# Optimization experiments

Measured on AMD Instinct MI355X. Metric: run time of the kernel, lower is better.

Reference implementation:

```python
import jax, jax.numpy as jnp
import numpy as np

B, L, E = 512, 50, 512
VOCAB = 32000
EPS = 1e-5


def setup_inputs() -> dict:
    key = jax.random.key(0)
    ks = jax.random.split(key, 16)
    inp = {
        'src_tokens': jax.random.randint(ks[0], (B, L), 0, VOCAB, dtype=jnp.int32),
        'trg_tokens': jax.random.randint(ks[1], (B, L), 0, VOCAB, dtype=jnp.int32),
        'pad_idx': 1,
        'emb_src': jax.random.normal(ks[2], (VOCAB, E), jnp.float32) * 0.02,
        'emb_trg': jax.random.normal(ks[3], (VOCAB, E), jnp.float32) * 0.02,
        'W1': jax.random.normal(ks[4], (20, E), jnp.float32) / np.sqrt(E),  # Conv1d(1,20,k=E) kernel squeezed
        'b1': jax.random.normal(ks[5], (20,), jnp.float32) * 0.01,
        'g1': jnp.ones((20,), jnp.float32),
        'beta1': jnp.zeros((20,), jnp.float32),
        'W2': jax.random.normal(ks[6], (40, 20, 3, 3), jnp.float32) / np.sqrt(20 * 9),
        'b2': jax.random.normal(ks[7], (40,), jnp.float32) * 0.01,
        'g2': jnp.ones((40,), jnp.float32),
        'beta2': jnp.zeros((40,), jnp.float32),
        'Wfc1': jax.random.normal(ks[8], (20, 40 * 11 * 11), jnp.float32) / np.sqrt(40 * 11 * 11),
        'bfc1': jnp.zeros((20,), jnp.float32),
        'Wfc2': jax.random.normal(ks[9], (1, 20), jnp.float32) / np.sqrt(20),
        'bfc2': jnp.zeros((1,), jnp.float32),
    }
    return inp


def _maxpool2(x):  # [B,C,H,W] -> 2x2/2 valid max pool
    return jax.lax.reduce_window(x, -jnp.inf, jax.lax.max, (1, 1, 2, 2), (1, 1, 2, 2), 'VALID')


def reference(src_tokens, trg_tokens, pad_idx, emb_src, emb_trg, W1, b1, g1, beta1,
              W2, b2, g2, beta2, Wfc1, bfc1, Wfc2, bfc2):
    src_e = emb_src[src_tokens]  # [B,L,E]
    trg_e = emb_trg[trg_tokens]  # [B,L,E]

    def conv1_bn_relu(x):
        # per-sample Conv1d(1,20,k=E): collapses E -> scalar per position/channel
        f = jnp.einsum('ble,ce->blc', x, W1) + b1  # [B,L,20]
        # per-sample BatchNorm1d in training mode: stats over the L positions of each sample
        mu = jnp.mean(f, axis=1, keepdims=True)
        var = jnp.var(f, axis=1, keepdims=True)  # biased, as torch uses for normalization
        f = (f - mu) * jax.lax.rsqrt(var + EPS) * g1 + beta1
        return jax.nn.relu(f)

    s = conv1_bn_relu(src_e)  # [B,L,20]
    t = conv1_bn_relu(trg_e)  # [B,L,20]

    # broadcast outer-sum: out[b,i,j,c] = s[b,j,c] + t[b,i,c]
    out = s[:, None, :, :] + t[:, :, None, :]          # [B,L,L,20]
    out = jnp.transpose(out, (0, 3, 1, 2))             # [B,20,L,L]
    out = _maxpool2(out)                                # [B,20,25,25]

    out = jax.lax.conv_general_dilated(out, W2, (1, 1), 'VALID') + b2[None, :, None, None]  # [B,40,23,23]
    # BatchNorm2d training mode: stats over (batch, H, W)
    mu = jnp.mean(out, axis=(0, 2, 3), keepdims=True)
    var = jnp.var(out, axis=(0, 2, 3), keepdims=True)
    out = (out - mu) * jax.lax.rsqrt(var + EPS) * g2[None, :, None, None] + beta2[None, :, None, None]
    out = jax.nn.relu(out)
    out = _maxpool2(out)                                # [B,40,11,11]

    out = out.reshape(out.shape[0], -1)                 # [B,4840]
    out = out @ Wfc1.T + bfc1
    out = out @ Wfc2.T + bfc2
    return jax.nn.sigmoid(out)                          # [B,1]
```

## Files before the change

### kernel.cpp

```cpp
#include <hip/hip_runtime.h>
#include <hip/hip_bf16.h>

#define EPS 1e-5f

__device__ __forceinline__ float bf2f(unsigned short u) {
  union { unsigned int i; float f; } x; x.i = ((unsigned int)u) << 16; return x.f;
}
__device__ __forceinline__ float loadp(const void* p, int i, bool f32) {
  return f32 ? ((const float*)p)[i] : bf2f(((const unsigned short*)p)[i]);
}
__device__ __forceinline__ bool detect_f32(const void* g1) {
  return ((const unsigned int*)g1)[0] == 0x3F800000u;
}

__global__ __launch_bounds__(256) void k0_prep(
    const void* __restrict__ W1, const void* __restrict__ W2,
    const void* __restrict__ Wfc1,
    const void* __restrict__ g1, const void* __restrict__ beta1,
    const void* __restrict__ g2, const void* __restrict__ beta2,
    const void* __restrict__ bfc1, const void* __restrict__ Wfc2,
    const void* __restrict__ bfc2,
    float* __restrict__ W1T, float* __restrict__ WT, float* __restrict__ WS,
    float* __restrict__ Wfc1T, float* __restrict__ prm)
{
  const bool f32 = detect_f32(g1);
  int g = blockIdx.x * 256 + threadIdx.x;
  const int NT = 64 * 256;
  for (int i = g; i < 512 * 20; i += NT) {
    int e = i / 20, c = i - e * 20;
    W1T[i] = loadp(W1, c * 512 + e, f32);
  }
  for (int i = g; i < 40 * 3 * 20; i += NT) {
    int o = i / 60, r = i - o * 60;
    int k = r / 20, c = r - k * 20;
    float st = 0.f, ss = 0.f;
    for (int q = 0; q < 3; ++q) {
      st += loadp(W2, ((o * 20 + c) * 3 + k) * 3 + q, f32);
      ss += loadp(W2, ((o * 20 + c) * 3 + q) * 3 + k, f32);
    }
    WT[(o * 3 + k) * 20 + c] = st;
    WS[(o * 3 + k) * 20 + c] = ss;
  }
  for (int i = g; i < 4840 * 20; i += NT) {
    int kk = i / 4840, idx = i - kk * 4840;
    Wfc1T[idx * 20 + kk] = loadp(Wfc1, i, f32);
  }
  if (g < 20)        prm[g] = loadp(g1,    g,       f32);
  else if (g < 40)   prm[g] = loadp(beta1, g - 20,  f32);
  else if (g < 80)   prm[g] = loadp(g2,    g - 40,  f32);
  else if (g < 120)  prm[g] = loadp(beta2, g - 80,  f32);
  else if (g < 140)  prm[g] = loadp(bfc1,  g - 120, f32);
  else if (g < 160)  prm[g] = loadp(Wfc2,  g - 140, f32);
  else if (g == 160) prm[g] = loadp(bfc2,  0,       f32);
}

__global__ __launch_bounds__(512) void k12_fused(
    const int* __restrict__ src_tok, const int* __restrict__ trg_tok,
    const void* __restrict__ emb_src, const void* __restrict__ emb_trg,
    const void* __restrict__ g1flag,
    const float* __restrict__ W1T,
    const float* __restrict__ WT, const float* __restrict__ WS,
    const float* __restrict__ prm,
    float* __restrict__ C1, float* __restrict__ R, float* __restrict__ S2)
{
  __shared__ float part[8 * 64 * 21];
  __shared__ float fl[1000];
  __shared__ float wl[2400];
  __shared__ float pmax[500];
  __shared__ float convl[40 * 24];
  __shared__ float sc[20], sh[20];
  const bool f32 = detect_f32(g1flag);
  int bb = blockIdx.x;
  int side = bb >> 9, b = bb & 511;
  int t = threadIdx.x;
  int lane = t & 63;
  int ch = __builtin_amdgcn_readfirstlane(t >> 6);

  float acc[20];
#pragma unroll
  for (int c = 0; c < 20; ++c) acc[c] = 0.f;
  if (lane < 50) {
    int tok = side ? trg_tok[b * 50 + lane] : src_tok[b * 50 + lane];
    const void* emb = side ? emb_trg : emb_src;
    if (f32) {
      const float4* rowp = (const float4*)((const float*)emb + (size_t)tok * 512 + ch * 64);
      for (int half = 0; half < 2; ++half) {
        float4 u[8];
#pragma unroll
        for (int q = 0; q < 8; ++q) u[q] = rowp[half * 8 + q];
#pragma unroll
        for (int q = 0; q < 8; ++q) {
          float v[4] = { u[q].x, u[q].y, u[q].z, u[q].w };
          const float* w = W1T + (ch * 64 + half * 32 + q * 4) * 20;
#pragma unroll
          for (int j = 0; j < 4; ++j)
#pragma unroll
            for (int c = 0; c < 20; ++c) acc[c] = fmaf(v[j], w[j * 20 + c], acc[c]);
        }
      }
    } else {
      const uint4* rowp = (const uint4*)((const unsigned short*)emb + (size_t)tok * 512 + ch * 64);
      uint4 u[8];
#pragma unroll
      for (int q = 0; q < 8; ++q) u[q] = rowp[q];
#pragma unroll
      for (int q = 0; q < 8; ++q) {
        const unsigned int* qu = (const unsigned int*)&u[q];
        float v[8];
#pragma unroll
        for (int j = 0; j < 4; ++j) {
          union { unsigned int i; float f; } lo, hi;
          lo.i = qu[j] << 16; hi.i = qu[j] & 0xffff0000u;
          v[2 * j] = lo.f; v[2 * j + 1] = hi.f;
        }
        const float* w = W1T + (ch * 64 + q * 8) * 20;
#pragma unroll
        for (int j = 0; j < 8; ++j)
#pragma unroll
          for (int c = 0; c < 20; ++c) acc[c] = fmaf(v[j], w[j * 20 + c], acc[c]);
      }
    }
    float* pp = &part[(ch * 64 + lane) * 21];
#pragma unroll
    for (int c = 0; c < 20; ++c) pp[c] = acc[c];
  }
  {
    const float* wsrc = side ? WT : WS;
    for (int i = t; i < 2400; i += 512) wl[i] = wsrc[i];
  }
  __syncthreads();
  for (int i = t; i < 1000; i += 512) {
    int l = i / 20, c = i - l * 20;
    float s = 0.f;
#pragma unroll
    for (int c2 = 0; c2 < 8; ++c2) s += part[(c2 * 64 + l) * 21 + c];
    fl[i] = s;
  }
  __syncthreads();
  if (t < 20) {
    float s = 0.f, s2 = 0.f;
#pragma unroll
    for (int l = 0; l < 50; ++l) { float v = fl[l * 20 + t]; s += v; s2 += v * v; }
    float mu = s * (1.0f / 50.0f);
    float var = s2 * (1.0f / 50.0f) - mu * mu;
    float k = prm[t] * rsqrtf(var + EPS);
    sc[t] = k; sh[t] = prm[20 + t] - k * mu;
  }
  __syncthreads();
  for (int i = t; i < 500; i += 512) {
    int p = i / 20, c = i - p * 20;
    float k = sc[c], s0 = sh[c];
    float v0 = fmaxf(k * fl[(2 * p) * 20 + c] + s0, 0.f);
    float v1 = fmaxf(k * fl[(2 * p + 1) * 20 + c] + s0, 0.f);
    pmax[i] = fmaxf(v0, v1);
  }
  __syncthreads();
  for (int i = t; i < 920; i += 512) {
    int o = i / 23, y = i - o * 23;
    float a = 0.f;
#pragma unroll
    for (int ky = 0; ky < 3; ++ky) {
      const float* wr = &wl[(o * 3 + ky) * 20];
      const float* pr = &pmax[(y + ky) * 20];
#pragma unroll
      for (int c = 0; c < 20; ++c) a = fmaf(wr[c], pr[c], a);
    }
    C1[((size_t)o * 1024 + bb) * 23 + y] = a;
    convl[o * 24 + y] = a;
  }
  __syncthreads();
  if (t < 40) {
    float s = 0.f, s2 = 0.f;
#pragma unroll
    for (int y = 0; y < 23; ++y) { float v = convl[t * 24 + y]; s += v; s2 += v * v; }
    R[t * 1024 + bb] = s;
    S2[t * 1024 + bb] = s2;
  }
}

__global__ __launch_bounds__(256) void k3_bn2(
    const float* __restrict__ R, const float* __restrict__ S2,
    const float* __restrict__ prm,
    float* __restrict__ bn2)
{
  int o = blockIdx.x, t = threadIdx.x;
  float s1a = 0, s2a = 0, s1b = 0, s2b = 0, sab = 0;
  for (int b = t; b < 512; b += 256) {
    float ra = R[o * 1024 + 512 + b], rb = R[o * 1024 + b];
    s1a += ra; s1b += rb; sab += ra * rb;
    s2a += S2[o * 1024 + 512 + b];
    s2b += S2[o * 1024 + b];
  }
  __shared__ float Rd[5][256];
  Rd[0][t] = s1a; Rd[1][t] = s2a; Rd[2][t] = s1b; Rd[3][t] = s2b; Rd[4][t] = sab;
  __syncthreads();
  for (int s = 128; s > 0; s >>= 1) {
    if (t < s) {
#pragma unroll
      for (int q = 0; q < 5; ++q) Rd[q][t] += Rd[q][t + s];
    }
    __syncthreads();
  }
  if (t == 0) {
    const float invN = 1.0f / (512.0f * 23.0f);
    float muA = Rd[0][0] * invN, muB = Rd[2][0] * invN;
    float ea2 = Rd[1][0] * invN - muA * muA;
    float eb2 = Rd[3][0] * invN - muB * muB;
    float cross = 2.0f * (Rd[4][0] * (1.0f / (529.0f * 512.0f)) - muA * muB);
    float var = ea2 + eb2 + cross;
    float k = prm[40 + o] * rsqrtf(var + EPS);
    bn2[o] = k;
    bn2[40 + o] = prm[80 + o] - k * (muA + muB);
  }
}

__global__ __launch_bounds__(256) void k4_fc(
    const float* __restrict__ C1,
    const float* __restrict__ bn2,
    const float* __restrict__ Wfc1T,
    const float* __restrict__ prm,
    const void* __restrict__ g1flag,
    void* __restrict__ outv)
{
  const bool f32 = detect_f32(g1flag);
  int b = blockIdx.x, t = threadIdx.x;
  __shared__ float mA[440], mB[440];
  __shared__ float k2s[40], c2s[40];
  __shared__ float red[20][256];
  __shared__ float o1[20];
  if (t < 40) k2s[t] = bn2[t];
  else if (t < 80) c2s[t - 40] = bn2[t];
  __syncthreads();
  for (int i = t; i < 440; i += 256) {
    int o = i / 11, y = i - o * 11;
    const float* pa = C1 + ((size_t)o * 1024 + 512 + b) * 23;
    const float* pb = C1 + ((size_t)o * 1024 + b) * 23;
    float a0 = pa[2 * y], a1 = pa[2 * y + 1];
    float b0 = pb[2 * y], b1 = pb[2 * y + 1];
    if (k2s[o] >= 0.f) { mA[i] = fmaxf(a0, a1); mB[i] = fmaxf(b0, b1); }
    else               { mA[i] = fminf(a0, a1); mB[i] = fminf(b0, b1); }
  }
  __syncthreads();
  float acc[20];
#pragma unroll
  for (int c = 0; c < 20; ++c) acc[c] = 0.f;
  for (int idx = t; idx < 4840; idx += 256) {
    int o = idx / 121, r = idx - o * 121;
    int y = r / 11, x = r - y * 11;
    float p = fmaxf(k2s[o] * (mA[o * 11 + y] + mB[o * 11 + x]) + c2s[o], 0.f);
    const float* w = Wfc1T + idx * 20;
#pragma unroll
    for (int c = 0; c < 20; ++c) acc[c] = fmaf(p, w[c], acc[c]);
  }
#pragma unroll
  for (int c = 0; c < 20; ++c) red[c][t] = acc[c];
  __syncthreads();
  for (int s = 128; s > 0; s >>= 1) {
    if (t < s) {
#pragma unroll
      for (int c = 0; c < 20; ++c) red[c][t] += red[c][t + s];
    }
    __syncthreads();
  }
  if (t < 20) o1[t] = red[t][0] + prm[120 + t];
  __syncthreads();
  if (t == 0) {
    float z = prm[160];
#pragma unroll
    for (int c = 0; c < 20; ++c) z = fmaf(prm[140 + c], o1[c], z);
    float sg = 1.0f / (1.0f + expf(-z));
    if (f32) ((float*)outv)[b] = sg;
    else     ((__hip_bfloat16*)outv)[b] = __float2bfloat16(sg);
  }
}

extern "C" void kernel_launch(void* const* d_in, const int* in_sizes, int n_in,
                              void* d_out, int out_size, void* d_ws, size_t ws_size,
                              hipStream_t stream) {
  const int* src_tok = (const int*)d_in[0];
  const int* trg_tok = (const int*)d_in[1];
  const void* emb_src = d_in[3];
  const void* emb_trg = d_in[4];
  const void* W1    = d_in[5];
  const void* g1    = d_in[7];
  const void* beta1 = d_in[8];
  const void* W2    = d_in[9];
  const void* g2    = d_in[11];
  const void* beta2 = d_in[12];
  const void* Wfc1  = d_in[13];
  const void* bfc1  = d_in[14];
  const void* Wfc2  = d_in[15];
  const void* bfc2  = d_in[16];

  char* ws = (char*)d_ws;
  float* W1T   = (float*)(ws + 0);
  float* WT    = (float*)(ws + 40960);
  float* WS    = (float*)(ws + 50560);
  float* Wfc1T = (float*)(ws + 60160);
  float* prm   = (float*)(ws + 447360);
  float* bn2   = (float*)(ws + 448384);
  float* R     = (float*)(ws + 448896);
  float* S2    = (float*)(ws + 612736);
  float* C1    = (float*)(ws + 776576);

  k0_prep<<<64, 256, 0, stream>>>(W1, W2, Wfc1, g1, beta1, g2, beta2, bfc1, Wfc2,
                                  bfc2, W1T, WT, WS, Wfc1T, prm);
  k12_fused<<<1024, 512, 0, stream>>>(src_tok, trg_tok, emb_src, emb_trg, g1,
                                      W1T, WT, WS, prm, C1, R, S2);
  k3_bn2<<<40, 256, 0, stream>>>(R, S2, prm, bn2);
  k4_fc<<<512, 256, 0, stream>>>(C1, bn2, Wfc1T, prm, g1, d_out);
}
```

Measured before the change: 202.8 us.

## Use bf16 MFMA for embedding-conv projection and halve block size

Adds a bf16 path that computes the embedding-by-W1 projection with 32x32x16 MFMA instructions, using a pre-packed W1 fragment buffer built in the prep kernel. The block shrinks from 512 to 256 threads. The f32 path is restructured so each of 4 waves handles 128 embedding elements, with a two-stage shared-memory reduction. The MFMA path targets the scalar FMA cost of the bf16 case. The f32 path trades parallelism per block for lower reduction and sync overhead.

```diff
diff --git a/kernel.cpp b/kernel.cpp
--- a/kernel.cpp
+++ b/kernel.cpp
@@ -2,6 +2,9 @@
 #include <hip/hip_bf16.h>
 
 #define EPS 1e-5f
+
+typedef __attribute__((ext_vector_type(8)))  short bf16x8;
+typedef __attribute__((ext_vector_type(16))) float f32x16;
 
 __device__ __forceinline__ float bf2f(unsigned short u) {
   union { unsigned int i; float f; } x; x.i = ((unsigned int)u) << 16; return x.f;
@@ -21,7 +24,8 @@
     const void* __restrict__ bfc1, const void* __restrict__ Wfc2,
     const void* __restrict__ bfc2,
     float* __restrict__ W1T, float* __restrict__ WT, float* __restrict__ WS,
-    float* __restrict__ Wfc1T, float* __restrict__ prm)
+    float* __restrict__ Wfc1T, float* __restrict__ prm,
+    unsigned short* __restrict__ Bp)
 {
   const bool f32 = detect_f32(g1);
   int g = blockIdx.x * 256 + threadIdx.x;
@@ -30,6 +34,16 @@
     int e = i / 20, c = i - e * 20;
     W1T[i] = loadp(W1, c * 512 + e, f32);
   }
+  const unsigned short* W1u = (const unsigned short*)W1;
+  for (int i = g; i < 2048; i += NT) {
+    int s = i >> 6, lane = i & 63;
+    int n = lane & 31, hk = lane >> 5;
+#pragma unroll
+    for (int j = 0; j < 8; ++j) {
+      int e = s * 16 + hk * 8 + j;
+      Bp[i * 8 + j] = (n < 20) ? W1u[n * 512 + e] : (unsigned short)0;
+    }
+  }
   for (int i = g; i < 40 * 3 * 20; i += NT) {
     int o = i / 60, r = i - o * 60;
     int k = r / 20, c = r - k * 20;
@@ -54,16 +68,17 @@
   else if (g == 160) prm[g] = loadp(bfc2,  0,       f32);
 }
 
-__global__ __launch_bounds__(512) void k12_fused(
+__global__ __launch_bounds__(256) void k12_fused(
     const int* __restrict__ src_tok, const int* __restrict__ trg_tok,
     const void* __restrict__ emb_src, const void* __restrict__ emb_trg,
     const void* __restrict__ g1flag,
     const float* __restrict__ W1T,
+    const unsigned short* __restrict__ Bp,
     const float* __restrict__ WT, const float* __restrict__ WS,
     const float* __restrict__ prm,
     float* __restrict__ C1, float* __restrict__ R, float* __restrict__ S2)
 {
-  __shared__ float part[8 * 64 * 21];
+  __shared__ float part[4 * 64 * 17];
   __shared__ float fl[1000];
   __shared__ float wl[2400];
   __shared__ float pmax[500];
@@ -74,69 +89,101 @@
   int side = bb >> 9, b = bb & 511;
   int t = threadIdx.x;
   int lane = t & 63;
-  int ch = __builtin_amdgcn_readfirstlane(t >> 6);
-
-  float acc[20];
-#pragma unroll
-  for (int c = 0; c < 20; ++c) acc[c] = 0.f;
-  if (lane < 50) {
-    int tok = side ? trg_tok[b * 50 + lane] : src_tok[b * 50 + lane];
-    const void* emb = side ? emb_trg : emb_src;
-    if (f32) {
-      const float4* rowp = (const float4*)((const float*)emb + (size_t)tok * 512 + ch * 64);
-      for (int half = 0; half < 2; ++half) {
+  int wave = __builtin_amdgcn_readfirstlane(t >> 6);
+
+  {
+    const float* wsrc = side ? WT : WS;
+    for (int i = t; i < 2400; i += 256) wl[i] = wsrc[i];
+  }
+
+  if (!f32) {
+    int tile = wave >> 1, kh = wave & 1;
+    int m = lane & 31, half = lane >> 5;
+    int grow = tile * 32 + m;
+    int lrow = grow < 50 ? grow : 49;
+    int tok = side ? trg_tok[b * 50 + lrow] : src_tok[b * 50 + lrow];
+    const unsigned short* arow =
+        (const unsigned short*)(side ? emb_trg : emb_src) + (size_t)tok * 512 + half * 8;
+    const unsigned short* bbase = Bp + ((size_t)(kh * 16) * 64 + lane) * 8;
+    f32x16 acc;
+#pragma unroll
+    for (int r = 0; r < 16; ++r) acc[r] = 0.f;
+    int s0 = kh * 16;
+#pragma unroll
+    for (int batch = 0; batch < 4; ++batch) {
+      uint4 ua[4], ub[4];
+#pragma unroll
+      for (int r = 0; r < 4; ++r) {
+        int s = s0 + batch * 4 + r;
+        ua[r] = *(const uint4*)(arow + s * 16);
+        ub[r] = *(const uint4*)(bbase + (batch * 4 + r) * 512);
+      }
+#pragma unroll
+      for (int r = 0; r < 4; ++r) {
+        union { uint4 u; bf16x8 h; } a, bfr;
+        a.u = ua[r]; bfr.u = ub[r];
+        acc = __builtin_amdgcn_mfma_f32_32x32x16_bf16(a.h, bfr.h, acc, 0, 0, 0);
+      }
+    }
+    float* pp = &part[wave * 1088 + lane * 17];
+#pragma unroll
+    for (int r = 0; r < 16; ++r) pp[r] = acc[r];
+    __syncthreads();
+    if (t < 128) {
+      int tl = t >> 6, ln = t & 63;
+      int c = ln & 31;
+#pragma unroll
+      for (int reg = 0; reg < 16; ++reg) {
+        float v = part[(tl * 2) * 1088 + ln * 17 + reg] +
+                  part[(tl * 2 + 1) * 1088 + ln * 17 + reg];
+        int row = (reg & 3) + 8 * (reg >> 2) + 4 * (ln >> 5);
+        int gr = tl * 32 + row;
+        if (c < 20 && gr < 50) fl[gr * 20 + c] = v;
+      }
+    }
+    __syncthreads();
+  } else {
+    float acc[20];
+#pragma unroll
+    for (int c = 0; c < 20; ++c) acc[c] = 0.f;
+    if (lane < 50) {
+      int tok = side ? trg_tok[b * 50 + lane] : src_tok[b * 50 + lane];
+      const float4* rowp = (const float4*)((const float*)(side ? emb_trg : emb_src) +
+                                           (size_t)tok * 512 + wave * 128);
+      for (int q8 = 0; q8 < 4; ++q8) {
         float4 u[8];
 #pragma unroll
-        for (int q = 0; q < 8; ++q) u[q] = rowp[half * 8 + q];
+        for (int q = 0; q < 8; ++q) u[q] = rowp[q8 * 8 + q];
 #pragma unroll
         for (int q = 0; q < 8; ++q) {
           float v[4] = { u[q].x, u[q].y, u[q].z, u[q].w };
-          const float* w = W1T + (ch * 64 + half * 32 + q * 4) * 20;
+          const float* w = W1T + (wave * 128 + q8 * 32 + q * 4) * 20;
 #pragma unroll
           for (int j = 0; j < 4; ++j)
 #pragma unroll
             for (int c = 0; c < 20; ++c) acc[c] = fmaf(v[j], w[j * 20 + c], acc[c]);
         }
       }
-    } else {
-      const uint4* rowp = (const uint4*)((const unsigned short*)emb + (size_t)tok * 512 + ch * 64);
-      uint4 u[8];
-#pragma unroll
-      for (int q = 0; q < 8; ++q) u[q] = rowp[q];
-#pragma unroll
-      for (int q = 0; q < 8; ++q) {
-        const unsigned int* qu = (const unsigned int*)&u[q];
-        float v[8];
-#pragma unroll
-        for (int j = 0; j < 4; ++j) {
-          union { unsigned int i; float f; } lo, hi;
-          lo.i = qu[j] << 16; hi.i = qu[j] & 0xffff0000u;
-          v[2 * j] = lo.f; v[2 * j + 1] = hi.f;
-        }
-        const float* w = W1T + (ch * 64 + q * 8) * 20;
-#pragma unroll
-        for (int j = 0; j < 8; ++j)
-#pragma unroll
-          for (int c = 0; c < 20; ++c) acc[c] = fmaf(v[j], w[j * 20 + c], acc[c]);
-      }
-    }
-    float* pp = &part[(ch * 64 + lane) * 21];
-#pragma unroll
-    for (int c = 0; c < 20; ++c) pp[c] = acc[c];
-  }
-  {
-    const float* wsrc = side ? WT : WS;
-    for (int i = t; i < 2400; i += 512) wl[i] = wsrc[i];
-  }
-  __syncthreads();
-  for (int i = t; i < 1000; i += 512) {
-    int l = i / 20, c = i - l * 20;
-    float s = 0.f;
-#pragma unroll
-    for (int c2 = 0; c2 < 8; ++c2) s += part[(c2 * 64 + l) * 21 + c];
-    fl[i] = s;
-  }
-  __syncthreads();
+    }
+    if (wave < 2 && lane < 50) {
+      float* pp = &part[(wave * 64 + lane) * 21];
+#pragma unroll
+      for (int c = 0; c < 20; ++c) pp[c] = acc[c];
+    }
+    __syncthreads();
+    if (wave >= 2 && lane < 50) {
+      float* pp = &part[((wave - 2) * 64 + lane) * 21];
+#pragma unroll
+      for (int c = 0; c < 20; ++c) pp[c] += acc[c];
+    }
+    __syncthreads();
+    for (int i = t; i < 1000; i += 256) {
+      int l = i / 20, c = i - l * 20;
+      fl[i] = part[(l) * 21 + c] + part[(64 + l) * 21 + c];
+    }
+    __syncthreads();
+  }
+
   if (t < 20) {
     float s = 0.f, s2 = 0.f;
 #pragma unroll
@@ -147,15 +194,15 @@
     sc[t] = k; sh[t] = prm[20 + t] - k * mu;
   }
   __syncthreads();
-  for (int i = t; i < 500; i += 512) {
+  for (int i = t; i < 500; i += 256) {
     int p = i / 20, c = i - p * 20;
-    float k = sc[c], s0 = sh[c];
-    float v0 = fmaxf(k * fl[(2 * p) * 20 + c] + s0, 0.f);
-    float v1 = fmaxf(k * fl[(2 * p + 1) * 20 + c] + s0, 0.f);
+    float k = sc[c], s0v = sh[c];
+    float v0 = fmaxf(k * fl[(2 * p) * 20 + c] + s0v, 0.f);
+    float v1 = fmaxf(k * fl[(2 * p + 1) * 20 + c] + s0v, 0.f);
     pmax[i] = fmaxf(v0, v1);
   }
   __syncthreads();
-  for (int i = t; i < 920; i += 512) {
+  for (int i = t; i < 920; i += 256) {
     int o = i / 23, y = i - o * 23;
     float a = 0.f;
 #pragma unroll
@@ -293,20 +340,21 @@
   const void* bfc2  = d_in[16];
 
   char* ws = (char*)d_ws;
-  float* W1T   = (float*)(ws + 0);
-  float* WT    = (float*)(ws + 40960);
-  float* WS    = (float*)(ws + 50560);
-  float* Wfc1T = (float*)(ws + 60160);
-  float* prm   = (float*)(ws + 447360);
-  float* bn2   = (float*)(ws + 448384);
-  float* R     = (float*)(ws + 448896);
-  float* S2    = (float*)(ws + 612736);
-  float* C1    = (float*)(ws + 776576);
+  float* W1T          = (float*)(ws + 0);
+  float* WT           = (float*)(ws + 40960);
+  float* WS           = (float*)(ws + 50560);
+  float* Wfc1T        = (float*)(ws + 60160);
+  float* prm          = (float*)(ws + 447360);
+  float* bn2          = (float*)(ws + 448384);
+  float* R            = (float*)(ws + 448896);
+  float* S2           = (float*)(ws + 612736);
+  unsigned short* Bp  = (unsigned short*)(ws + 776576);
+  float* C1           = (float*)(ws + 809344);
 
   k0_prep<<<64, 256, 0, stream>>>(W1, W2, Wfc1, g1, beta1, g2, beta2, bfc1, Wfc2,
-                                  bfc2, W1T, WT, WS, Wfc1T, prm);
-  k12_fused<<<1024, 512, 0, stream>>>(src_tok, trg_tok, emb_src, emb_trg, g1,
-                                      W1T, WT, WS, prm, C1, R, S2);
+                                  bfc2, W1T, WT, WS, Wfc1T, prm, Bp);
+  k12_fused<<<1024, 256, 0, stream>>>(src_tok, trg_tok, emb_src, emb_trg, g1,
+                                      W1T, Bp, WT, WS, prm, C1, R, S2);
   k3_bn2<<<40, 256, 0, stream>>>(R, S2, prm, bn2);
   k4_fc<<<512, 256, 0, stream>>>(C1, bn2, Wfc1T, prm, g1, d_out);
 }
```

Result: slower. 215.8 us (+6.4%).

## Precompute conv1 projection for whole vocabulary, then gather per token

Applied to the files above, without the earlier changes.

Splits the fused kernel in two. The first projects every row of both embedding tables through W1 into a compact bf16 table with 24-element rows. The second gathers those 20-value rows per token instead of gathering full 512-wide embedding rows and reducing them per sample. This trades random full-row gathers and partially idle lanes for a fully streaming pass over both tables. That pass touches more rows in total (the full vocabulary rather than only the tokens used) and rounds the projected features to bf16, which adds precision loss.

```diff
diff --git a/kernel.cpp b/kernel.cpp
--- a/kernel.cpp
+++ b/kernel.cpp
@@ -54,87 +54,113 @@
   else if (g == 160) prm[g] = loadp(bfc2,  0,       f32);
 }
 
-__global__ __launch_bounds__(512) void k12_fused(
-    const int* __restrict__ src_tok, const int* __restrict__ trg_tok,
+__global__ __launch_bounds__(256) void k1_vocab(
     const void* __restrict__ emb_src, const void* __restrict__ emb_trg,
     const void* __restrict__ g1flag,
     const float* __restrict__ W1T,
+    unsigned short* __restrict__ F)
+{
+  __shared__ float part[128 * 21];
+  const bool f32 = detect_f32(g1flag);
+  int t = threadIdx.x;
+  int slot = t & 127;
+  int kh = __builtin_amdgcn_readfirstlane(t >> 7);
+  int grow = blockIdx.x * 128 + slot;
+  int table = grow >= 32000;
+  int v = grow - table * 32000;
+  const void* emb = table ? emb_trg : emb_src;
+  float acc[20];
+#pragma unroll
+  for (int c = 0; c < 20; ++c) acc[c] = 0.f;
+  if (!f32) {
+    const uint4* rowp = (const uint4*)((const unsigned short*)emb + (size_t)v * 512 + kh * 256);
+    for (int outer = 0; outer < 4; ++outer) {
+      uint4 u[8];
+#pragma unroll
+      for (int q = 0; q < 8; ++q) u[q] = rowp[outer * 8 + q];
+#pragma unroll
+      for (int q = 0; q < 8; ++q) {
+        const unsigned int* qu = (const unsigned int*)&u[q];
+        float vv[8];
+#pragma unroll
+        for (int j = 0; j < 4; ++j) {
+          union { unsigned int i; float f; } lo, hi;
+          lo.i = qu[j] << 16; hi.i = qu[j] & 0xffff0000u;
+          vv[2 * j] = lo.f; vv[2 * j + 1] = hi.f;
+        }
+        const float* w = W1T + (kh * 256 + outer * 64 + q * 8) * 20;
+#pragma unroll
+        for (int j = 0; j < 8; ++j)
+#pragma unroll
+          for (int c = 0; c < 20; ++c) acc[c] = fmaf(vv[j], w[j * 20 + c], acc[c]);
+      }
+    }
+  } else {
+    const float4* rowp = (const float4*)((const float*)emb + (size_t)v * 512 + kh * 256);
+    for (int outer = 0; outer < 8; ++outer) {
+      float4 u[8];
+#pragma unroll
+      for (int q = 0; q < 8; ++q) u[q] = rowp[outer * 8 + q];
+#pragma unroll
+      for (int q = 0; q < 8; ++q) {
+        float vv[4] = { u[q].x, u[q].y, u[q].z, u[q].w };
+        const float* w = W1T + (kh * 256 + outer * 32 + q * 4) * 20;
+#pragma unroll
+        for (int j = 0; j < 4; ++j)
+#pragma unroll
+          for (int c = 0; c < 20; ++c) acc[c] = fmaf(vv[j], w[j * 20 + c], acc[c]);
+      }
+    }
+  }
+  if (kh == 0) {
+    float* pp = &part[slot * 21];
+#pragma unroll
+    for (int c = 0; c < 20; ++c) pp[c] = acc[c];
+  }
+  __syncthreads();
+  if (kh == 1) {
+    float* pp = &part[slot * 21];
+#pragma unroll
+    for (int c = 0; c < 20; ++c) pp[c] += acc[c];
+  }
+  __syncthreads();
+  for (int i = t; i < 2560; i += 256) {
+    int row = i / 20, c = i - row * 20;
+    float val = part[row * 21 + c];
+    F[(size_t)(blockIdx.x * 128 + row) * 24 + c] =
+        (unsigned short)(__bfloat16_as_ushort(__float2bfloat16(val)));
+  }
+}
+
+__global__ __launch_bounds__(256) void k2_sample(
+    const int* __restrict__ src_tok, const int* __restrict__ trg_tok,
+    const unsigned short* __restrict__ F,
     const float* __restrict__ WT, const float* __restrict__ WS,
     const float* __restrict__ prm,
     float* __restrict__ C1, float* __restrict__ R, float* __restrict__ S2)
 {
-  __shared__ float part[8 * 64 * 21];
   __shared__ float fl[1000];
   __shared__ float wl[2400];
   __shared__ float pmax[500];
   __shared__ float convl[40 * 24];
   __shared__ float sc[20], sh[20];
-  const bool f32 = detect_f32(g1flag);
+  __shared__ int tokl[50];
   int bb = blockIdx.x;
   int side = bb >> 9, b = bb & 511;
   int t = threadIdx.x;
-  int lane = t & 63;
-  int ch = __builtin_amdgcn_readfirstlane(t >> 6);
-
-  float acc[20];
-#pragma unroll
-  for (int c = 0; c < 20; ++c) acc[c] = 0.f;
-  if (lane < 50) {
-    int tok = side ? trg_tok[b * 50 + lane] : src_tok[b * 50 + lane];
-    const void* emb = side ? emb_trg : emb_src;
-    if (f32) {
-      const float4* rowp = (const float4*)((const float*)emb + (size_t)tok * 512 + ch * 64);
-      for (int half = 0; half < 2; ++half) {
-        float4 u[8];
-#pragma unroll
-        for (int q = 0; q < 8; ++q) u[q] = rowp[half * 8 + q];
-#pragma unroll
-        for (int q = 0; q < 8; ++q) {
-          float v[4] = { u[q].x, u[q].y, u[q].z, u[q].w };
-          const float* w = W1T + (ch * 64 + half * 32 + q * 4) * 20;
-#pragma unroll
-          for (int j = 0; j < 4; ++j)
-#pragma unroll
-            for (int c = 0; c < 20; ++c) acc[c] = fmaf(v[j], w[j * 20 + c], acc[c]);
-        }
-      }
-    } else {
-      const uint4* rowp = (const uint4*)((const unsigned short*)emb + (size_t)tok * 512 + ch * 64);
-      uint4 u[8];
-#pragma unroll
-      for (int q = 0; q < 8; ++q) u[q] = rowp[q];
-#pragma unroll
-      for (int q = 0; q < 8; ++q) {
-        const unsigned int* qu = (const unsigned int*)&u[q];
-        float v[8];
-#pragma unroll
-        for (int j = 0; j < 4; ++j) {
-          union { unsigned int i; float f; } lo, hi;
-          lo.i = qu[j] << 16; hi.i = qu[j] & 0xffff0000u;
-          v[2 * j] = lo.f; v[2 * j + 1] = hi.f;
-        }
-        const float* w = W1T + (ch * 64 + q * 8) * 20;
-#pragma unroll
-        for (int j = 0; j < 8; ++j)
-#pragma unroll
-          for (int c = 0; c < 20; ++c) acc[c] = fmaf(v[j], w[j * 20 + c], acc[c]);
-      }
-    }
-    float* pp = &part[(ch * 64 + lane) * 21];
-#pragma unroll
-    for (int c = 0; c < 20; ++c) pp[c] = acc[c];
-  }
-  {
-    const float* wsrc = side ? WT : WS;
-    for (int i = t; i < 2400; i += 512) wl[i] = wsrc[i];
-  }
-  __syncthreads();
-  for (int i = t; i < 1000; i += 512) {
-    int l = i / 20, c = i - l * 20;
-    float s = 0.f;
-#pragma unroll
-    for (int c2 = 0; c2 < 8; ++c2) s += part[(c2 * 64 + l) * 21 + c];
-    fl[i] = s;
+  if (t < 50) tokl[t] = side ? trg_tok[b * 50 + t] : src_tok[b * 50 + t];
+  const float* wsrc = side ? WT : WS;
+  for (int i = t; i < 2400; i += 256) wl[i] = wsrc[i];
+  __syncthreads();
+  if (t < 250) {
+    int l = t / 5, j = t - (t / 5) * 5;
+    const unsigned short* fr = F + (size_t)(side * 32000 + tokl[l]) * 24 + j * 4;
+    uint2 u = *(const uint2*)fr;
+    union { unsigned int i; float f; } e0, e1, e2, e3;
+    e0.i = u.x << 16; e1.i = u.x & 0xffff0000u;
+    e2.i = u.y << 16; e3.i = u.y & 0xffff0000u;
+    float* dst = &fl[l * 20 + j * 4];
+    dst[0] = e0.f; dst[1] = e1.f; dst[2] = e2.f; dst[3] = e3.f;
   }
   __syncthreads();
   if (t < 20) {
@@ -147,7 +173,7 @@
     sc[t] = k; sh[t] = prm[20 + t] - k * mu;
   }
   __syncthreads();
-  for (int i = t; i < 500; i += 512) {
+  for (int i = t; i < 500; i += 256) {
     int p = i / 20, c = i - p * 20;
     float k = sc[c], s0 = sh[c];
     float v0 = fmaxf(k * fl[(2 * p) * 20 + c] + s0, 0.f);
@@ -155,7 +181,7 @@
     pmax[i] = fmaxf(v0, v1);
   }
   __syncthreads();
-  for (int i = t; i < 920; i += 512) {
+  for (int i = t; i < 920; i += 256) {
     int o = i / 23, y = i - o * 23;
     float a = 0.f;
 #pragma unroll
@@ -293,20 +319,21 @@
   const void* bfc2  = d_in[16];
 
   char* ws = (char*)d_ws;
-  float* W1T   = (float*)(ws + 0);
-  float* WT    = (float*)(ws + 40960);
-  float* WS    = (float*)(ws + 50560);
-  float* Wfc1T = (float*)(ws + 60160);
-  float* prm   = (float*)(ws + 447360);
-  float* bn2   = (float*)(ws + 448384);
-  float* R     = (float*)(ws + 448896);
-  float* S2    = (float*)(ws + 612736);
-  float* C1    = (float*)(ws + 776576);
+  float* W1T          = (float*)(ws + 0);
+  float* WT           = (float*)(ws + 40960);
+  float* WS           = (float*)(ws + 50560);
+  float* Wfc1T        = (float*)(ws + 60160);
+  float* prm          = (float*)(ws + 447360);
+  float* bn2          = (float*)(ws + 448384);
+  float* R            = (float*)(ws + 448896);
+  float* S2           = (float*)(ws + 612736);
+  unsigned short* F   = (unsigned short*)(ws + 776576);
+  float* C1           = (float*)(ws + 3848576);
 
   k0_prep<<<64, 256, 0, stream>>>(W1, W2, Wfc1, g1, beta1, g2, beta2, bfc1, Wfc2,
                                   bfc2, W1T, WT, WS, Wfc1T, prm);
-  k12_fused<<<1024, 512, 0, stream>>>(src_tok, trg_tok, emb_src, emb_trg, g1,
-                                      W1T, WT, WS, prm, C1, R, S2);
+  k1_vocab<<<500, 256, 0, stream>>>(emb_src, emb_trg, g1, W1T, F);
+  k2_sample<<<1024, 256, 0, stream>>>(src_tok, trg_tok, F, WT, WS, prm, C1, R, S2);
   k3_bn2<<<40, 256, 0, stream>>>(R, S2, prm, bn2);
   k4_fc<<<512, 256, 0, stream>>>(C1, bn2, Wfc1T, prm, g1, d_out);
 }
```

Result: slower. 221.6 us (+9.3%).
